# Optimization experiments

Hardware: AMD Instinct MI355X
Metric: run time of the kernel (lower is better)

The kernel has to match this reference:

```python
import jax, jax.numpy as jnp
import numpy as np

EPS = 1e-5        # torch LayerNorm default eps
INNER = 4
AFFECT_W = 0.3
BATCH = 65536
DIM = 128


def _ln(x, g, b):
    m = jnp.mean(x, axis=-1, keepdims=True)
    v = jnp.var(x, axis=-1, keepdims=True)
    return (x - m) * jax.lax.rsqrt(v + EPS) * g + b


def _gelu(x):
    return jax.nn.gelu(x, approximate=False)  # torch nn.GELU default (erf)


def setup_inputs() -> dict:
    key = jax.random.key(0)
    ks = jax.random.split(key, 18)
    B, d = BATCH, DIM

    def W(k, i, o):
        return jax.random.normal(k, (i, o), jnp.float32) / np.float32(np.sqrt(i))

    return {
        "x": jax.random.normal(ks[0], (B, d), jnp.float32),
        "y_init": jax.random.normal(ks[1], (B, d), jnp.float32),
        "affect_vec": jax.random.normal(ks[2], (B, 3), jnp.float32),
        "ln_latent_g": jnp.ones((3 * d,), jnp.float32), "ln_latent_b": jnp.zeros((3 * d,), jnp.float32),
        "ln_answer_g": jnp.ones((2 * d,), jnp.float32), "ln_answer_b": jnp.zeros((2 * d,), jnp.float32),
        "ln_z_g": jnp.ones((d,), jnp.float32), "ln_z_b": jnp.zeros((d,), jnp.float32),
        "lat_w1": W(ks[3], 3 * d, 2 * d), "lat_b1": jnp.zeros((2 * d,), jnp.float32),
        "lat_w2": W(ks[4], 2 * d, d), "lat_b2": jnp.zeros((d,), jnp.float32),
        "ans_w1": W(ks[5], 2 * d, 2 * d), "ans_b1": jnp.zeros((2 * d,), jnp.float32),
        "ans_w2": W(ks[6], 2 * d, d), "ans_b2": jnp.zeros((d,), jnp.float32),
        "aff_w": W(ks[7], 3, d), "aff_b": jnp.zeros((d,), jnp.float32),
        "gate_w": W(ks[8], 2 * d, 1), "gate_b": jnp.zeros((1,), jnp.float32),
        "q_w": W(ks[9], d, d), "q_b": jnp.zeros((d,), jnp.float32),
        "k_w": W(ks[10], d, d), "k_b": jnp.zeros((d,), jnp.float32),
        "v_w": W(ks[11], d, d), "v_b": jnp.zeros((d,), jnp.float32),
        "o_w": W(ks[12], d, d), "o_b": jnp.zeros((d,), jnp.float32),
        "pad_w1": W(ks[13], d, d // 2), "pad_b1": jnp.zeros((d // 2,), jnp.float32),
        "pad_w2": W(ks[14], d // 2, 3), "pad_b2": jnp.zeros((3,), jnp.float32),
        "K": 5,
    }


def _forward(x, y_init, affect_vec, ln_latent_g, ln_latent_b, ln_answer_g, ln_answer_b,
             ln_z_g, ln_z_b, lat_w1, lat_b1, lat_w2, lat_b2, ans_w1, ans_b1, ans_w2, ans_b2,
             aff_w, aff_b, gate_w, gate_b, q_w, q_b, k_w, k_b, v_w, v_b, o_w, o_b,
             pad_w1, pad_b1, pad_w2, pad_b2, K):
    d = x.shape[-1]
    scale = jnp.float32(d) ** -0.5
    y = y_init
    z = jnp.zeros_like(y)
    confs = []     # scalar gate means (detached, like .item() in torch)
    history = []   # list of [B, 1, d] z snapshots
    memory = []    # SoulKernel memory buffer: list of [d] rinse_state[0] snapshots
    for _ in range(K):
        for _ in range(INNER):
            li = _ln(jnp.concatenate([x, y, z], axis=-1), ln_latent_g, ln_latent_b)
            z_delta = _gelu(li @ lat_w1 + lat_b1) @ lat_w2 + lat_b2
            z = _ln(z + 0.3 * z_delta, ln_z_g, ln_z_b)
        affect_latent = jnp.tanh(affect_vec @ aff_w + aff_b)          # [B, d]
        gate = jax.nn.sigmoid(jnp.concatenate([z, affect_latent], axis=-1) @ gate_w + gate_b)  # [B, 1]
        z = z + AFFECT_W * gate * affect_latent
        confs.append(jax.lax.stop_gradient(jnp.mean(gate)))
        history.append(z[:, None, :])
        if len(history) > 1:
            seq = jnp.concatenate(history, axis=1)  # [B, t, d]
            Q = seq @ q_w + q_b
            Kt = seq @ k_w + k_b
            V = seq @ v_w + v_b
            attn = jax.nn.softmax(jnp.einsum('bsd,btd->bst', Q, Kt) * scale, axis=-1)
            attn_out = jnp.einsum('bst,btd->bsd', attn, V) @ o_w + o_b
            z = _ln(z + attn_out[:, -1, :], ln_z_g, ln_z_b)
        rinse = jnp.tanh(z + y)
        # SoulKernel (hope is computed but unused in the original)
        faith = jnp.sqrt(sum(confs) / len(confs))
        z = z + faith * 0.05 * z
        future = jnp.mean(jnp.stack(memory[-3:]), axis=0) if memory else jnp.zeros((d,), x.dtype)  # [d]
        bond = jnp.tanh(jax.lax.stop_gradient(jnp.mean(x * z)) + jax.lax.stop_gradient(jnp.mean(y * rinse)))
        z = z + 0.2 * bond * (future - z)
        rinse = jnp.tanh(rinse + future * 0.3)
        memory.append(jax.lax.stop_gradient(rinse[0]))
        ai = _ln(jnp.concatenate([y, z], axis=-1), ln_answer_g, ln_answer_b)
        y = y + 0.4 * (_gelu(ai @ ans_w1 + ans_b1) @ ans_w2 + ans_b2)
    pad = jnp.tanh(_gelu(z @ pad_w1 + pad_b1) @ pad_w2 + pad_b2)
    return y, jnp.stack(confs), pad


def reference(x, y_init, affect_vec, ln_latent_g, ln_latent_b, ln_answer_g, ln_answer_b,
              ln_z_g, ln_z_b, lat_w1, lat_b1, lat_w2, lat_b2, ans_w1, ans_b1, ans_w2, ans_b2,
              aff_w, aff_b, gate_w, gate_b, q_w, q_b, k_w, k_b, v_w, v_b, o_w, o_b,
              pad_w1, pad_b1, pad_w2, pad_b2, K):
    return _forward(x, y_init, affect_vec, ln_latent_g, ln_latent_b, ln_answer_g, ln_answer_b,
                    ln_z_g, ln_z_b, lat_w1, lat_b1, lat_w2, lat_b2, ans_w1, ans_b1, ans_w2, ans_b2,
                    aff_w, aff_b, gate_w, gate_b, q_w, q_b, k_w, k_b, v_w, v_b, o_w, o_b,
                    pad_w1, pad_b1, pad_w2, pad_b2, K)
```

## Files before the change

### kernel.cpp

```cpp
#include <hip/hip_runtime.h>
#include <math.h>


#define BATCH 65536
#define D 128
#define BD ((size_t)BATCH * D)
#define NSTEP 5
#define ROWS 32
#define NTHR 256
#define NBLK (BATCH / ROWS)
#define LN_EPS 1e-5f
#define ATT_SCALE 0.08838834764831845f
#define LDA 132
#define LDB 260

#define WS_Z    ((size_t)0)
#define WS_H1   (BD)
#define WS_PART (WS_H1 + 5*BD)
#define WS_SCAL (WS_PART + (size_t)NBLK*4)
#define WS_H2   (WS_SCAL + 2048)
#define WS_KV_END (WS_H2 + 5*BD)

#define SC_FS   0
#define SC_B02  1
#define SC_CSUM 2
#define SC_FUT  16
#define SC_MEM  256
#define SC_R10  960

struct Args {
  const float *x, *y_init, *affect;
  const float *g_lat, *b_lat, *g_ans, *b_ans, *g_z, *b_z;
  const float *lw1, *lb1, *lw2, *lb2;
  const float *aw1, *ab1, *aw2, *ab2;
  const float *affw, *affb, *gw, *gb;
  const float *qw, *qb, *kw, *kb, *vw, *vb, *ow, *ob;
  const float *pw1, *pb1, *pw2, *pb2;
  float *Y, *conf, *pad;
  float *Z, *H1, *H2, *PART, *SCAL;
  int useKV;
};

__device__ __forceinline__ float4 ld4(const float* p) { return *(const float4*)p; }
__device__ __forceinline__ void st4(float* p, float4 v) { *(float4*)p = v; }
__device__ __forceinline__ float geluf(float v) { return 0.5f*v*(1.0f + erff(v*0.70710678118654752f)); }
__device__ __forceinline__ float dot4(float4 a, float4 b){ return a.x*b.x + a.y*b.y + a.z*b.z + a.w*b.w; }
__device__ __forceinline__ void accSQ(float4 v, float& S, float& Q) {
  S += v.x+v.y+v.z+v.w;
  Q += v.x*v.x + v.y*v.y + v.z*v.z + v.w*v.w;
}

template<int KDIM, int NPT>
__device__ __forceinline__ void mm_block(const float* __restrict__ W, int N,
                                         const float* As, int lda,
                                         int rg, int cg, float (&acc)[4][NPT])
{
  const float* a0 = As + (rg*4+0)*lda;
  const float* a1 = As + (rg*4+1)*lda;
  const float* a2 = As + (rg*4+2)*lda;
  const float* a3 = As + (rg*4+3)*lda;
  const float* wp = W + cg*NPT;
  #pragma unroll 4
  for (int k = 0; k < KDIM; ++k) {
    float w[NPT];
    if constexpr (NPT == 8) {
      float4 w0 = ld4(wp + (size_t)k*N);
      float4 w1 = ld4(wp + (size_t)k*N + 4);
      w[0]=w0.x; w[1]=w0.y; w[2]=w0.z; w[3]=w0.w;
      w[4]=w1.x; w[5]=w1.y; w[6]=w1.z; w[7]=w1.w;
    } else if constexpr (NPT == 4) {
      float4 w0 = ld4(wp + (size_t)k*N);
      w[0]=w0.x; w[1]=w0.y; w[2]=w0.z; w[3]=w0.w;
    } else {
      float2 w0 = *(const float2*)(wp + (size_t)k*N);
      w[0]=w0.x; w[1]=w0.y;
    }
    float av0=a0[k], av1=a1[k], av2=a2[k], av3=a3[k];
    #pragma unroll
    for (int c = 0; c < NPT; ++c) {
      acc[0][c] += av0*w[c];
      acc[1][c] += av1*w[c];
      acc[2][c] += av2*w[c];
      acc[3][c] += av3*w[c];
    }
  }
}

__device__ __forceinline__ void z_ln_update(const Args& A, int row0, int rg, int cg,
                                            const float (&add)[4][4])
{
  float4 g4 = ld4(A.g_z + cg*4);
  float4 b4 = ld4(A.b_z + cg*4);
  #pragma unroll
  for (int rr = 0; rr < 4; ++rr) {
    size_t off = (size_t)(row0 + rg*4 + rr)*D + cg*4;
    float4 z = ld4(A.Z + off);
    float v0 = z.x + add[rr][0];
    float v1 = z.y + add[rr][1];
    float v2 = z.z + add[rr][2];
    float v3 = z.w + add[rr][3];
    float S = v0+v1+v2+v3;
    float Q = v0*v0+v1*v1+v2*v2+v3*v3;
    S += __shfl_xor(S,1);  Q += __shfl_xor(Q,1);
    S += __shfl_xor(S,2);  Q += __shfl_xor(Q,2);
    S += __shfl_xor(S,4);  Q += __shfl_xor(Q,4);
    S += __shfl_xor(S,8);  Q += __shfl_xor(Q,8);
    S += __shfl_xor(S,16); Q += __shfl_xor(Q,16);
    float m  = S*(1.f/128.f);
    float rs = rsqrtf(Q*(1.f/128.f) - m*m + LN_EPS);
    float4 o;
    o.x = (v0-m)*rs*g4.x + b4.x;
    o.y = (v1-m)*rs*g4.y + b4.y;
    o.z = (v2-m)*rs*g4.z + b4.z;
    o.w = (v3-m)*rs*g4.w + b4.w;
    st4(A.Z + off, o);
  }
}

__device__ __forceinline__ void stage_raw(float* sA, const float* src, int row0, int t)
{
  for (int e4 = t; e4 < ROWS*32; e4 += NTHR) {
    int r = e4 >> 5, c4 = e4 & 31;
    st4(sA + r*LDA + c4*4, ld4(src + (size_t)(row0+r)*D + c4*4));
  }
}

__device__ __forceinline__ void epilogue_phase(const Args& A, float* sB, float* sM, float* sR,
                                               int row0, int t, int rg, int cg, int r8, int sub)
{
  const float fs  = A.SCAL[SC_FS];
  const float b02 = A.SCAL[SC_B02];
  const float a   = fs*(1.0f - b02);
  for (int e4 = t; e4 < ROWS*32; e4 += NTHR) {
    int r = e4 >> 5, c4 = e4 & 31;
    size_t off = (size_t)(row0 + r)*D + c4*4;
    float4 z = ld4(A.Z + off);
    float4 f = ld4(A.SCAL + SC_FUT + c4*4);
    z.x = z.x*a + b02*f.x;
    z.y = z.y*a + b02*f.y;
    z.z = z.z*a + b02*f.z;
    z.w = z.w*a + b02*f.w;
    st4(A.Z + off, z);
  }
  __syncthreads();
  {
    const float* yr = A.Y + (size_t)(row0 + r8)*D;
    const float* zr = A.Z + (size_t)(row0 + r8)*D;
    float S = 0.f, Q = 0.f;
    #pragma unroll
    for (int j = 0; j < 4; ++j) {
      int c = (sub + 8*j)*4;
      accSQ(ld4(yr + c), S, Q);
      accSQ(ld4(zr + c), S, Q);
    }
    S += __shfl_xor(S,1); Q += __shfl_xor(Q,1);
    S += __shfl_xor(S,2); Q += __shfl_xor(Q,2);
    S += __shfl_xor(S,4); Q += __shfl_xor(Q,4);
    if (sub == 0) {
      float m = S*(1.f/256.f);
      sM[r8] = m;
      sR[r8] = rsqrtf(Q*(1.f/256.f) - m*m + LN_EPS);
    }
  }
  __syncthreads();
  for (int e4 = t; e4 < ROWS*64; e4 += NTHR) {
    int r = e4 >> 6, c4 = e4 & 63;
    int k = c4*4;
    float m = sM[r], rs = sR[r];
    float4 v = (k < D) ? ld4(A.Y + (size_t)(row0+r)*D + k)
                       : ld4(A.Z + (size_t)(row0+r)*D + (k - D));
    float4 g = ld4(A.g_ans + k);
    float4 b = ld4(A.b_ans + k);
    float4 o;
    o.x = (v.x-m)*rs*g.x + b.x;
    o.y = (v.y-m)*rs*g.y + b.y;
    o.z = (v.z-m)*rs*g.z + b.z;
    o.w = (v.w-m)*rs*g.w + b.w;
    st4(sB + r*LDB + k, o);
  }
  __syncthreads();
  float acc[4][8] = {};
  mm_block<256,8>(A.aw1, 256, sB, LDB, rg, cg, acc);
  float4 b1a = ld4(A.ab1 + cg*8);
  float4 b1b = ld4(A.ab1 + cg*8 + 4);
  float h[4][8];
  #pragma unroll
  for (int rr = 0; rr < 4; ++rr) {
    h[rr][0]=geluf(acc[rr][0]+b1a.x); h[rr][1]=geluf(acc[rr][1]+b1a.y);
    h[rr][2]=geluf(acc[rr][2]+b1a.z); h[rr][3]=geluf(acc[rr][3]+b1a.w);
    h[rr][4]=geluf(acc[rr][4]+b1b.x); h[rr][5]=geluf(acc[rr][5]+b1b.y);
    h[rr][6]=geluf(acc[rr][6]+b1b.z); h[rr][7]=geluf(acc[rr][7]+b1b.w);
  }
  __syncthreads();
  #pragma unroll
  for (int rr = 0; rr < 4; ++rr) {
    float4 h0; h0.x=h[rr][0]; h0.y=h[rr][1]; h0.z=h[rr][2]; h0.w=h[rr][3];
    float4 h1; h1.x=h[rr][4]; h1.y=h[rr][5]; h1.z=h[rr][6]; h1.w=h[rr][7];
    st4(sB + (rg*4+rr)*LDB + cg*8,     h0);
    st4(sB + (rg*4+rr)*LDB + cg*8 + 4, h1);
  }
  __syncthreads();
  float acc2[4][4] = {};
  mm_block<256,4>(A.aw2, 128, sB, LDB, rg, cg, acc2);
  float4 b2 = ld4(A.ab2 + cg*4);
  #pragma unroll
  for (int rr = 0; rr < 4; ++rr) {
    size_t off = (size_t)(row0 + rg*4 + rr)*D + cg*4;
    float4 y = ld4(A.Y + off);
    y.x += 0.4f*(acc2[rr][0] + b2.x);
    y.y += 0.4f*(acc2[rr][1] + b2.y);
    y.z += 0.4f*(acc2[rr][2] + b2.z);
    y.w += 0.4f*(acc2[rr][3] + b2.w);
    st4(A.Y + off, y);
  }
  __syncthreads();
}

__global__ void prepK(Args A)
{
  size_t i  = (size_t)blockIdx.x*blockDim.x + threadIdx.x;
  size_t n4 = BD/4;
  float4 zero; zero.x=0.f; zero.y=0.f; zero.z=0.f; zero.w=0.f;
  for (; i < n4; i += (size_t)gridDim.x*blockDim.x) {
    ((float4*)A.Z)[i] = zero;
    ((float4*)A.Y)[i] = ((const float4*)A.y_init)[i];
  }
}

template<int STEP>
__global__ __launch_bounds__(NTHR, 2) void stepK(Args A)
{
  __shared__ __align__(16) float sA[ROWS*LDA];
  __shared__ __align__(16) float sB[ROWS*LDB];
  __shared__ float sM[ROWS], sR[ROWS], sG[ROWS];
  __shared__ float sS[ROWS][8];
  __shared__ float sRed[4][2];

  const int t = threadIdx.x;
  const int row0 = blockIdx.x * ROWS;
  const int rg = t >> 5, cg = t & 31;
  const int r8 = t >> 3, sub = t & 7;

  if (STEP > 0)
    epilogue_phase(A, sB, sM, sR, row0, t, rg, cg, r8, sub);

  #pragma unroll 1
  for (int it = 0; it < 4; ++it) {
    {
      const float* xr = A.x + (size_t)(row0 + r8)*D;
      const float* yr = A.Y + (size_t)(row0 + r8)*D;
      const float* zr = A.Z + (size_t)(row0 + r8)*D;
      float S = 0.f, Q = 0.f;
      #pragma unroll
      for (int j = 0; j < 4; ++j) {
        int c = (sub + 8*j)*4;
        accSQ(ld4(xr + c), S, Q);
        accSQ(ld4(yr + c), S, Q);
        accSQ(ld4(zr + c), S, Q);
      }
      S += __shfl_xor(S,1); Q += __shfl_xor(Q,1);
      S += __shfl_xor(S,2); Q += __shfl_xor(Q,2);
      S += __shfl_xor(S,4); Q += __shfl_xor(Q,4);
      if (sub == 0) {
        float m = S*(1.f/384.f);
        sM[r8] = m;
        sR[r8] = rsqrtf(Q*(1.f/384.f) - m*m + LN_EPS);
      }
    }
    __syncthreads();
    float acc[4][8] = {};
    #pragma unroll 1
    for (int seg = 0; seg < 3; ++seg) {
      const float* src = (seg == 0) ? A.x : (seg == 1 ? (const float*)A.Y : (const float*)A.Z);
      for (int e4 = t; e4 < ROWS*32; e4 += NTHR) {
        int r = e4 >> 5, c4 = e4 & 31;
        float4 v = ld4(src + (size_t)(row0+r)*D + c4*4);
        float m = sM[r], rs = sR[r];
        int k = seg*D + c4*4;
        float4 g = ld4(A.g_lat + k);
        float4 b = ld4(A.b_lat + k);
        float4 o;
        o.x = (v.x-m)*rs*g.x + b.x;
        o.y = (v.y-m)*rs*g.y + b.y;
        o.z = (v.z-m)*rs*g.z + b.z;
        o.w = (v.w-m)*rs*g.w + b.w;
        st4(sA + r*LDA + c4*4, o);
      }
      __syncthreads();
      mm_block<128,8>(A.lw1 + (size_t)seg*D*256, 256, sA, LDA, rg, cg, acc);
      __syncthreads();
    }
    float4 l1a = ld4(A.lb1 + cg*8);
    float4 l1b = ld4(A.lb1 + cg*8 + 4);
    #pragma unroll
    for (int rr = 0; rr < 4; ++rr) {
      float4 h0, h1;
      h0.x = geluf(acc[rr][0]+l1a.x); h0.y = geluf(acc[rr][1]+l1a.y);
      h0.z = geluf(acc[rr][2]+l1a.z); h0.w = geluf(acc[rr][3]+l1a.w);
      h1.x = geluf(acc[rr][4]+l1b.x); h1.y = geluf(acc[rr][5]+l1b.y);
      h1.z = geluf(acc[rr][6]+l1b.z); h1.w = geluf(acc[rr][7]+l1b.w);
      st4(sB + (rg*4+rr)*LDB + cg*8,     h0);
      st4(sB + (rg*4+rr)*LDB + cg*8 + 4, h1);
    }
    __syncthreads();
    float acc2[4][4] = {};
    mm_block<256,4>(A.lw2, 128, sB, LDB, rg, cg, acc2);
    float4 l2 = ld4(A.lb2 + cg*4);
    float add[4][4];
    #pragma unroll
    for (int rr = 0; rr < 4; ++rr) {
      add[rr][0] = 0.3f*(acc2[rr][0]+l2.x);
      add[rr][1] = 0.3f*(acc2[rr][1]+l2.y);
      add[rr][2] = 0.3f*(acc2[rr][2]+l2.z);
      add[rr][3] = 0.3f*(acc2[rr][3]+l2.w);
    }
    z_ln_update(A, row0, rg, cg, add);
    __syncthreads();
  }

  {
    size_t row = (size_t)row0 + r8;
    const float* zr = A.Z + row*D;
    float af0 = A.affect[row*3+0];
    float af1 = A.affect[row*3+1];
    float af2 = A.affect[row*3+2];
    float dg = 0.f;
    #pragma unroll
    for (int j = 0; j < 4; ++j) {
      int c = (sub + 8*j)*4;
      float4 zv = ld4(zr + c);
      float4 g1 = ld4(A.gw + c);
      float4 g2 = ld4(A.gw + D + c);
      float4 w0 = ld4(A.affw + c);
      float4 w1 = ld4(A.affw + D + c);
      float4 w2 = ld4(A.affw + 2*D + c);
      float4 ab = ld4(A.affb + c);
      float4 al;
      al.x = tanhf(af0*w0.x + af1*w1.x + af2*w2.x + ab.x);
      al.y = tanhf(af0*w0.y + af1*w1.y + af2*w2.y + ab.y);
      al.z = tanhf(af0*w0.z + af1*w1.z + af2*w2.z + ab.z);
      al.w = tanhf(af0*w0.w + af1*w1.w + af2*w2.w + ab.w);
      st4(sA + r8*LDA + c, al);
      dg += dot4(zv, g1) + dot4(al, g2);
    }
    dg += __shfl_xor(dg,1);
    dg += __shfl_xor(dg,2);
    dg += __shfl_xor(dg,4);
    if (sub == 0) sG[r8] = 1.f/(1.f + expf(-(dg + A.gb[0])));
  }
  __syncthreads();
  {
    float* zhw = A.H1 + (size_t)STEP*BD;
    for (int e4 = t; e4 < ROWS*32; e4 += NTHR) {
      int r = e4 >> 5, c4 = e4 & 31;
      size_t off = (size_t)(row0+r)*D + c4*4;
      float4 z  = ld4(A.Z + off);
      float4 al = ld4(sA + r*LDA + c4*4);
      float g = 0.3f * sG[r];
      z.x += g*al.x; z.y += g*al.y; z.z += g*al.z; z.w += g*al.w;
      st4(A.Z + off, z);
      if (!A.useKV) st4(zhw + off, z);
    }
  }
  __syncthreads();

  float q[4][4];
  if (A.useKV || STEP > 0) {
    stage_raw(sA, A.Z, row0, t);
    __syncthreads();
  }
  if (A.useKV) {
    float kacc[4][4] = {}, vacc[4][4] = {};
    mm_block<128,4>(A.kw, 128, sA, LDA, rg, cg, kacc);
    mm_block<128,4>(A.vw, 128, sA, LDA, rg, cg, vacc);
    float4 kb4 = ld4(A.kb + cg*4);
    float4 vb4 = ld4(A.vb + cg*4);
    float* KH = A.H1 + (size_t)STEP*BD;
    float* VH = A.H2 + (size_t)STEP*BD;
    #pragma unroll
    for (int rr = 0; rr < 4; ++rr) {
      size_t off = (size_t)(row0 + rg*4 + rr)*D + cg*4;
      float4 kv; kv.x=kacc[rr][0]+kb4.x; kv.y=kacc[rr][1]+kb4.y;
                 kv.z=kacc[rr][2]+kb4.z; kv.w=kacc[rr][3]+kb4.w;
      float4 vv; vv.x=vacc[rr][0]+vb4.x; vv.y=vacc[rr][1]+vb4.y;
                 vv.z=vacc[rr][2]+vb4.z; vv.w=vacc[rr][3]+vb4.w;
      st4(KH + off, kv);
      st4(VH + off, vv);
    }
  }
  if (STEP > 0) {
    float qacc[4][4] = {};
    mm_block<128,4>(A.qw, 128, sA, LDA, rg, cg, qacc);
    float4 qb4 = ld4(A.qb + cg*4);
    #pragma unroll
    for (int rr = 0; rr < 4; ++rr) {
      q[rr][0]=qacc[rr][0]+qb4.x; q[rr][1]=qacc[rr][1]+qb4.y;
      q[rr][2]=qacc[rr][2]+qb4.z; q[rr][3]=qacc[rr][3]+qb4.w;
    }
  }

  if (STEP > 0) {
    if (A.useKV) {
      #pragma unroll 1
      for (int j = 0; j <= STEP; ++j) {
        const float* KH = A.H1 + (size_t)j*BD;
        #pragma unroll
        for (int rr = 0; rr < 4; ++rr) {
          float4 kv = ld4(KH + (size_t)(row0 + rg*4 + rr)*D + cg*4);
          float s = q[rr][0]*kv.x + q[rr][1]*kv.y + q[rr][2]*kv.z + q[rr][3]*kv.w;
          s += __shfl_xor(s,1); s += __shfl_xor(s,2); s += __shfl_xor(s,4);
          s += __shfl_xor(s,8); s += __shfl_xor(s,16);
          if (cg == 0) sS[rg*4+rr][j] = s;
        }
      }
    } else {
      #pragma unroll 1
      for (int j = 0; j <= STEP; ++j) {
        __syncthreads();
        stage_raw(sA, A.H1 + (size_t)j*BD, row0, t);
        __syncthreads();
        float kacc[4][4] = {};
        mm_block<128,4>(A.kw, 128, sA, LDA, rg, cg, kacc);
        float4 kb4 = ld4(A.kb + cg*4);
        #pragma unroll
        for (int rr = 0; rr < 4; ++rr) {
          float s = q[rr][0]*(kacc[rr][0]+kb4.x) + q[rr][1]*(kacc[rr][1]+kb4.y)
                  + q[rr][2]*(kacc[rr][2]+kb4.z) + q[rr][3]*(kacc[rr][3]+kb4.w);
          s += __shfl_xor(s,1); s += __shfl_xor(s,2); s += __shfl_xor(s,4);
          s += __shfl_xor(s,8); s += __shfl_xor(s,16);
          if (cg == 0) sS[rg*4+rr][j] = s;
        }
      }
    }
    __syncthreads();
    if (t < ROWS) {
      float mx = -3.0e38f;
      for (int j = 0; j <= STEP; ++j) { float v = sS[t][j]*ATT_SCALE; sS[t][j] = v; mx = fmaxf(mx, v); }
      float sum = 0.f;
      for (int j = 0; j <= STEP; ++j) { float p = expf(sS[t][j]-mx); sS[t][j] = p; sum += p; }
      float inv = 1.f/sum;
      for (int j = 0; j <= STEP; ++j) sS[t][j] *= inv;
    }
    __syncthreads();
    float ao[4][4] = {};
    if (A.useKV) {
      #pragma unroll 1
      for (int j = 0; j <= STEP; ++j) {
        const float* VH = A.H2 + (size_t)j*BD;
        #pragma unroll
        for (int rr = 0; rr < 4; ++rr) {
          float p = sS[rg*4+rr][j];
          float4 vv = ld4(VH + (size_t)(row0 + rg*4 + rr)*D + cg*4);
          ao[rr][0] += p*vv.x; ao[rr][1] += p*vv.y;
          ao[rr][2] += p*vv.z; ao[rr][3] += p*vv.w;
        }
      }
    } else {
      #pragma unroll 1
      for (int j = 0; j <= STEP; ++j) {
        __syncthreads();
        stage_raw(sA, A.H1 + (size_t)j*BD, row0, t);
        __syncthreads();
        float vacc[4][4] = {};
        mm_block<128,4>(A.vw, 128, sA, LDA, rg, cg, vacc);
        float4 vb4 = ld4(A.vb + cg*4);
        #pragma unroll
        for (int rr = 0; rr < 4; ++rr) {
          float p = sS[rg*4+rr][j];
          ao[rr][0] += p*(vacc[rr][0]+vb4.x);
          ao[rr][1] += p*(vacc[rr][1]+vb4.y);
          ao[rr][2] += p*(vacc[rr][2]+vb4.z);
          ao[rr][3] += p*(vacc[rr][3]+vb4.w);
        }
      }
      __syncthreads();
    }
    #pragma unroll
    for (int rr = 0; rr < 4; ++rr) {
      float4 v; v.x=ao[rr][0]; v.y=ao[rr][1]; v.z=ao[rr][2]; v.w=ao[rr][3];
      st4(sA + (rg*4+rr)*LDA + cg*4, v);
    }
    __syncthreads();
    float oacc[4][4] = {};
    mm_block<128,4>(A.ow, 128, sA, LDA, rg, cg, oacc);
    float4 ob4 = ld4(A.ob + cg*4);
    float add[4][4];
    #pragma unroll
    for (int rr = 0; rr < 4; ++rr) {
      add[rr][0] = oacc[rr][0]+ob4.x;
      add[rr][1] = oacc[rr][1]+ob4.y;
      add[rr][2] = oacc[rr][2]+ob4.z;
      add[rr][3] = oacc[rr][3]+ob4.w;
    }
    z_ln_update(A, row0, rg, cg, add);
    __syncthreads();
  }

  {
    float sxz = 0.f, syr = 0.f;
    for (int e4 = t; e4 < ROWS*32; e4 += NTHR) {
      int r = e4 >> 5, c4 = e4 & 31;
      size_t off = (size_t)(row0+r)*D + c4*4;
      float4 xv = ld4(A.x + off);
      float4 zv = ld4(A.Z + off);
      float4 yv = ld4(A.Y + off);
      float4 rn;
      rn.x = tanhf(zv.x + yv.x);
      rn.y = tanhf(zv.y + yv.y);
      rn.z = tanhf(zv.z + yv.z);
      rn.w = tanhf(zv.w + yv.w);
      sxz += dot4(xv, zv);
      syr += dot4(yv, rn);
      if (blockIdx.x == 0 && r == 0)
        st4(A.SCAL + SC_R10 + c4*4, rn);
    }
    #pragma unroll
    for (int m2 = 1; m2 < 64; m2 <<= 1) { sxz += __shfl_xor(sxz,m2); syr += __shfl_xor(syr,m2); }
    if ((t & 63) == 0) { sRed[t>>6][0] = sxz; sRed[t>>6][1] = syr; }
    __syncthreads();
    if (t == 0) {
      float X = 0.f, Yv = 0.f, G = 0.f;
      #pragma unroll
      for (int w2 = 0; w2 < 4; ++w2) { X += sRed[w2][0]; Yv += sRed[w2][1]; }
      #pragma unroll
      for (int r = 0; r < ROWS; ++r) G += sG[r];
      float* p = A.PART + (size_t)blockIdx.x*4;
      p[0] = G; p[1] = X; p[2] = Yv;
    }
  }
}

template<int STEP>
__global__ void redK(Args A)
{
  __shared__ float sRed[4][3];
  const int t = threadIdx.x;
  float sg = 0.f, sxz = 0.f, syr = 0.f;
  for (int b = t; b < NBLK; b += 256) {
    const float* p = A.PART + (size_t)b*4;
    sg += p[0]; sxz += p[1]; syr += p[2];
  }
  #pragma unroll
  for (int m = 1; m < 64; m <<= 1) {
    sg  += __shfl_xor(sg,m);
    sxz += __shfl_xor(sxz,m);
    syr += __shfl_xor(syr,m);
  }
  if ((t & 63) == 0) { int w = t>>6; sRed[w][0]=sg; sRed[w][1]=sxz; sRed[w][2]=syr; }
  __syncthreads();
  if (t == 0) {
    float G=0.f, X=0.f, Yv=0.f;
    #pragma unroll
    for (int w = 0; w < 4; ++w) { G += sRed[w][0]; X += sRed[w][1]; Yv += sRed[w][2]; }
    float conf = G * (1.f/(float)BATCH);
    float csum = conf + (STEP == 0 ? 0.f : A.SCAL[SC_CSUM]);
    A.SCAL[SC_CSUM] = csum;
    A.conf[STEP] = conf;
    float faith = sqrtf(csum / (float)(STEP+1));
    float fs = 1.f + 0.05f*faith;
    float bond = tanhf((fs*X + Yv) * (1.f/((float)BATCH*(float)D)));
    A.SCAL[SC_FS]  = fs;
    A.SCAL[SC_B02] = 0.2f*bond;
  }
  if (t < D) {
    float fut = 0.f;
    if (STEP > 0) {
      int lo = (STEP-3 < 0) ? 0 : STEP-3;
      float s = 0.f;
      for (int j = lo; j < STEP; ++j) s += A.SCAL[SC_MEM + j*D + t];
      fut = s / (float)(STEP - lo);
    }
    A.SCAL[SC_FUT + t] = fut;
    A.SCAL[SC_MEM + STEP*D + t] = tanhf(A.SCAL[SC_R10 + t] + 0.3f*fut);
  }
}

__global__ __launch_bounds__(NTHR, 2) void finalK(Args A)
{
  __shared__ __align__(16) float sA[ROWS*LDA];
  __shared__ __align__(16) float sB[ROWS*LDB];
  __shared__ float sM[ROWS], sR[ROWS];
  const int t = threadIdx.x;
  const int row0 = blockIdx.x * ROWS;
  const int rg = t >> 5, cg = t & 31;
  const int r8 = t >> 3, sub = t & 7;

  epilogue_phase(A, sB, sM, sR, row0, t, rg, cg, r8, sub);

  stage_raw(sA, A.Z, row0, t);
  __syncthreads();
  float acc[4][2] = {};
  mm_block<128,2>(A.pw1, 64, sA, LDA, rg, cg, acc);
  float2 pb = *(const float2*)(A.pb1 + cg*2);
  #pragma unroll
  for (int rr = 0; rr < 4; ++rr) {
    sB[(rg*4+rr)*LDB + cg*2 + 0] = geluf(acc[rr][0] + pb.x);
    sB[(rg*4+rr)*LDB + cg*2 + 1] = geluf(acc[rr][1] + pb.y);
  }
  __syncthreads();
  {
    float o0=0.f, o1=0.f, o2=0.f;
    #pragma unroll
    for (int jj = 0; jj < 8; ++jj) {
      int j = sub*8 + jj;
      float p = sB[r8*LDB + j];
      o0 += p*A.pw2[j*3+0];
      o1 += p*A.pw2[j*3+1];
      o2 += p*A.pw2[j*3+2];
    }
    o0 += __shfl_xor(o0,1); o0 += __shfl_xor(o0,2); o0 += __shfl_xor(o0,4);
    o1 += __shfl_xor(o1,1); o1 += __shfl_xor(o1,2); o1 += __shfl_xor(o1,4);
    o2 += __shfl_xor(o2,1); o2 += __shfl_xor(o2,2); o2 += __shfl_xor(o2,4);
    if (sub == 0) {
      size_t ro = (size_t)(row0 + r8)*3;
      A.pad[ro+0] = tanhf(o0 + A.pb2[0]);
      A.pad[ro+1] = tanhf(o1 + A.pb2[1]);
      A.pad[ro+2] = tanhf(o2 + A.pb2[2]);
    }
  }
}

extern "C" void kernel_launch(void* const* d_in, const int* in_sizes, int n_in,
                              void* d_out, int out_size, void* d_ws, size_t ws_size,
                              hipStream_t stream)
{
  (void)in_sizes; (void)n_in; (void)out_size;
  Args a;
  a.x      = (const float*)d_in[0];
  a.y_init = (const float*)d_in[1];
  a.affect = (const float*)d_in[2];
  a.g_lat  = (const float*)d_in[3];
  a.b_lat  = (const float*)d_in[4];
  a.g_ans  = (const float*)d_in[5];
  a.b_ans  = (const float*)d_in[6];
  a.g_z    = (const float*)d_in[7];
  a.b_z    = (const float*)d_in[8];
  a.lw1    = (const float*)d_in[9];
  a.lb1    = (const float*)d_in[10];
  a.lw2    = (const float*)d_in[11];
  a.lb2    = (const float*)d_in[12];
  a.aw1    = (const float*)d_in[13];
  a.ab1    = (const float*)d_in[14];
  a.aw2    = (const float*)d_in[15];
  a.ab2    = (const float*)d_in[16];
  a.affw   = (const float*)d_in[17];
  a.affb   = (const float*)d_in[18];
  a.gw     = (const float*)d_in[19];
  a.gb     = (const float*)d_in[20];
  a.qw     = (const float*)d_in[21];
  a.qb     = (const float*)d_in[22];
  a.kw     = (const float*)d_in[23];
  a.kb     = (const float*)d_in[24];
  a.vw     = (const float*)d_in[25];
  a.vb     = (const float*)d_in[26];
  a.ow     = (const float*)d_in[27];
  a.ob     = (const float*)d_in[28];
  a.pw1    = (const float*)d_in[29];
  a.pb1    = (const float*)d_in[30];
  a.pw2    = (const float*)d_in[31];
  a.pb2    = (const float*)d_in[32];
  float* out = (float*)d_out;
  a.Y    = out;
  a.conf = out + BD;
  a.pad  = a.conf + NSTEP;
  float* ws = (float*)d_ws;
  a.Z    = ws + WS_Z;
  a.H1   = ws + WS_H1;
  a.PART = ws + WS_PART;
  a.SCAL = ws + WS_SCAL;
  a.H2   = ws + WS_H2;
  a.useKV = (ws_size >= WS_KV_END * sizeof(float)) ? 1 : 0;

  prepK<<<dim3(2048), dim3(256), 0, stream>>>(a);
  stepK<0><<<dim3(NBLK), dim3(NTHR), 0, stream>>>(a);
  redK<0><<<dim3(1), dim3(256), 0, stream>>>(a);
  stepK<1><<<dim3(NBLK), dim3(NTHR), 0, stream>>>(a);
  redK<1><<<dim3(1), dim3(256), 0, stream>>>(a);
  stepK<2><<<dim3(NBLK), dim3(NTHR), 0, stream>>>(a);
  redK<2><<<dim3(1), dim3(256), 0, stream>>>(a);
  stepK<3><<<dim3(NBLK), dim3(NTHR), 0, stream>>>(a);
  redK<3><<<dim3(1), dim3(256), 0, stream>>>(a);
  stepK<4><<<dim3(NBLK), dim3(NTHR), 0, stream>>>(a);
  redK<4><<<dim3(1), dim3(256), 0, stream>>>(a);
  finalK<<<dim3(NBLK), dim3(NTHR), 0, stream>>>(a);
}
```

Baseline: 8.319 ms.

## Split 256-wide shared tiles into two 128-wide halves, vectorize A loads, raise occupancy

The 256-column shared buffer sB (LDB=260) is replaced by two 128-column buffers sharing one stride, so 256-K matmuls run as two 128-K passes over sA and sB. This cuts shared memory per block, and the launch bounds rise from 2 to 4 blocks per CU. The matmul inner loop now reads activations as float4 over 4 k-steps, which reduces LDS instruction count. The tighter register budget from the higher occupancy target could cause spills in the 4x8 accumulator paths.

```diff
diff --git a/kernel.cpp b/kernel.cpp
--- a/kernel.cpp
+++ b/kernel.cpp
@@ -11,8 +11,7 @@
 #define NBLK (BATCH / ROWS)
 #define LN_EPS 1e-5f
 #define ATT_SCALE 0.08838834764831845f
-#define LDA 132
-#define LDB 260
+#define LDU 132
 
 #define WS_Z    ((size_t)0)
 #define WS_H1   (BD)
@@ -49,6 +48,9 @@
   S += v.x+v.y+v.z+v.w;
   Q += v.x*v.x + v.y*v.y + v.z*v.z + v.w*v.w;
 }
+__device__ __forceinline__ float getf(const float4& v, int i) {
+  return i==0 ? v.x : (i==1 ? v.y : (i==2 ? v.z : v.w));
+}
 
 template<int KDIM, int NPT>
 __device__ __forceinline__ void mm_block(const float* __restrict__ W, int N,
@@ -60,28 +62,36 @@
   const float* a2 = As + (rg*4+2)*lda;
   const float* a3 = As + (rg*4+3)*lda;
   const float* wp = W + cg*NPT;
-  #pragma unroll 4
-  for (int k = 0; k < KDIM; ++k) {
-    float w[NPT];
-    if constexpr (NPT == 8) {
-      float4 w0 = ld4(wp + (size_t)k*N);
-      float4 w1 = ld4(wp + (size_t)k*N + 4);
-      w[0]=w0.x; w[1]=w0.y; w[2]=w0.z; w[3]=w0.w;
-      w[4]=w1.x; w[5]=w1.y; w[6]=w1.z; w[7]=w1.w;
-    } else if constexpr (NPT == 4) {
-      float4 w0 = ld4(wp + (size_t)k*N);
-      w[0]=w0.x; w[1]=w0.y; w[2]=w0.z; w[3]=w0.w;
-    } else {
-      float2 w0 = *(const float2*)(wp + (size_t)k*N);
-      w[0]=w0.x; w[1]=w0.y;
-    }
-    float av0=a0[k], av1=a1[k], av2=a2[k], av3=a3[k];
-    #pragma unroll
-    for (int c = 0; c < NPT; ++c) {
-      acc[0][c] += av0*w[c];
-      acc[1][c] += av1*w[c];
-      acc[2][c] += av2*w[c];
-      acc[3][c] += av3*w[c];
+  #pragma unroll 2
+  for (int k4 = 0; k4 < KDIM/4; ++k4) {
+    float4 av0 = ld4(a0 + k4*4);
+    float4 av1 = ld4(a1 + k4*4);
+    float4 av2 = ld4(a2 + k4*4);
+    float4 av3 = ld4(a3 + k4*4);
+    #pragma unroll
+    for (int kk = 0; kk < 4; ++kk) {
+      const int k = k4*4 + kk;
+      float w[NPT];
+      if constexpr (NPT == 8) {
+        float4 w0 = ld4(wp + (size_t)k*N);
+        float4 w1 = ld4(wp + (size_t)k*N + 4);
+        w[0]=w0.x; w[1]=w0.y; w[2]=w0.z; w[3]=w0.w;
+        w[4]=w1.x; w[5]=w1.y; w[6]=w1.z; w[7]=w1.w;
+      } else if constexpr (NPT == 4) {
+        float4 w0 = ld4(wp + (size_t)k*N);
+        w[0]=w0.x; w[1]=w0.y; w[2]=w0.z; w[3]=w0.w;
+      } else {
+        float2 w0 = *(const float2*)(wp + (size_t)k*N);
+        w[0]=w0.x; w[1]=w0.y;
+      }
+      float e0 = getf(av0,kk), e1 = getf(av1,kk), e2 = getf(av2,kk), e3 = getf(av3,kk);
+      #pragma unroll
+      for (int c = 0; c < NPT; ++c) {
+        acc[0][c] += e0*w[c];
+        acc[1][c] += e1*w[c];
+        acc[2][c] += e2*w[c];
+        acc[3][c] += e3*w[c];
+      }
     }
   }
 }
@@ -121,11 +131,12 @@
 {
   for (int e4 = t; e4 < ROWS*32; e4 += NTHR) {
     int r = e4 >> 5, c4 = e4 & 31;
-    st4(sA + r*LDA + c4*4, ld4(src + (size_t)(row0+r)*D + c4*4));
-  }
-}
-
-__device__ __forceinline__ void epilogue_phase(const Args& A, float* sB, float* sM, float* sR,
+    st4(sA + r*LDU + c4*4, ld4(src + (size_t)(row0+r)*D + c4*4));
+  }
+}
+
+__device__ __forceinline__ void epilogue_phase(const Args& A, float* sA, float* sB,
+                                               float* sM, float* sR,
                                                int row0, int t, int rg, int cg, int r8, int sub)
 {
   const float fs  = A.SCAL[SC_FS];
@@ -176,11 +187,13 @@
     o.y = (v.y-m)*rs*g.y + b.y;
     o.z = (v.z-m)*rs*g.z + b.z;
     o.w = (v.w-m)*rs*g.w + b.w;
-    st4(sB + r*LDB + k, o);
+    float* base = (k < 128) ? sA : (sB - 128);
+    st4(base + r*LDU + k, o);
   }
   __syncthreads();
   float acc[4][8] = {};
-  mm_block<256,8>(A.aw1, 256, sB, LDB, rg, cg, acc);
+  mm_block<128,8>(A.aw1,                   256, sA, LDU, rg, cg, acc);
+  mm_block<128,8>(A.aw1 + (size_t)128*256, 256, sB, LDU, rg, cg, acc);
   float4 b1a = ld4(A.ab1 + cg*8);
   float4 b1b = ld4(A.ab1 + cg*8 + 4);
   float h[4][8];
@@ -192,16 +205,20 @@
     h[rr][6]=geluf(acc[rr][6]+b1b.z); h[rr][7]=geluf(acc[rr][7]+b1b.w);
   }
   __syncthreads();
-  #pragma unroll
-  for (int rr = 0; rr < 4; ++rr) {
-    float4 h0; h0.x=h[rr][0]; h0.y=h[rr][1]; h0.z=h[rr][2]; h0.w=h[rr][3];
-    float4 h1; h1.x=h[rr][4]; h1.y=h[rr][5]; h1.z=h[rr][6]; h1.w=h[rr][7];
-    st4(sB + (rg*4+rr)*LDB + cg*8,     h0);
-    st4(sB + (rg*4+rr)*LDB + cg*8 + 4, h1);
+  {
+    float* hb = (cg < 16) ? sA : (sB - 128);
+    #pragma unroll
+    for (int rr = 0; rr < 4; ++rr) {
+      float4 h0; h0.x=h[rr][0]; h0.y=h[rr][1]; h0.z=h[rr][2]; h0.w=h[rr][3];
+      float4 h1; h1.x=h[rr][4]; h1.y=h[rr][5]; h1.z=h[rr][6]; h1.w=h[rr][7];
+      st4(hb + (rg*4+rr)*LDU + cg*8,     h0);
+      st4(hb + (rg*4+rr)*LDU + cg*8 + 4, h1);
+    }
   }
   __syncthreads();
   float acc2[4][4] = {};
-  mm_block<256,4>(A.aw2, 128, sB, LDB, rg, cg, acc2);
+  mm_block<128,4>(A.aw2,                   128, sA, LDU, rg, cg, acc2);
+  mm_block<128,4>(A.aw2 + (size_t)128*128, 128, sB, LDU, rg, cg, acc2);
   float4 b2 = ld4(A.ab2 + cg*4);
   #pragma unroll
   for (int rr = 0; rr < 4; ++rr) {
@@ -228,10 +245,10 @@
 }
 
 template<int STEP>
-__global__ __launch_bounds__(NTHR, 2) void stepK(Args A)
-{
-  __shared__ __align__(16) float sA[ROWS*LDA];
-  __shared__ __align__(16) float sB[ROWS*LDB];
+__global__ __launch_bounds__(NTHR, 4) void stepK(Args A)
+{
+  __shared__ __align__(16) float sA[ROWS*LDU];
+  __shared__ __align__(16) float sB[ROWS*LDU];
   __shared__ float sM[ROWS], sR[ROWS], sG[ROWS];
   __shared__ float sS[ROWS][8];
   __shared__ float sRed[4][2];
@@ -242,7 +259,7 @@
   const int r8 = t >> 3, sub = t & 7;
 
   if (STEP > 0)
-    epilogue_phase(A, sB, sM, sR, row0, t, rg, cg, r8, sub);
+    epilogue_phase(A, sA, sB, sM, sR, row0, t, rg, cg, r8, sub);
 
   #pragma unroll 1
   for (int it = 0; it < 4; ++it) {
@@ -284,27 +301,31 @@
         o.y = (v.y-m)*rs*g.y + b.y;
         o.z = (v.z-m)*rs*g.z + b.z;
         o.w = (v.w-m)*rs*g.w + b.w;
-        st4(sA + r*LDA + c4*4, o);
+        st4(sA + r*LDU + c4*4, o);
       }
       __syncthreads();
-      mm_block<128,8>(A.lw1 + (size_t)seg*D*256, 256, sA, LDA, rg, cg, acc);
+      mm_block<128,8>(A.lw1 + (size_t)seg*D*256, 256, sA, LDU, rg, cg, acc);
       __syncthreads();
     }
     float4 l1a = ld4(A.lb1 + cg*8);
     float4 l1b = ld4(A.lb1 + cg*8 + 4);
-    #pragma unroll
-    for (int rr = 0; rr < 4; ++rr) {
-      float4 h0, h1;
-      h0.x = geluf(acc[rr][0]+l1a.x); h0.y = geluf(acc[rr][1]+l1a.y);
-      h0.z = geluf(acc[rr][2]+l1a.z); h0.w = geluf(acc[rr][3]+l1a.w);
-      h1.x = geluf(acc[rr][4]+l1b.x); h1.y = geluf(acc[rr][5]+l1b.y);
-      h1.z = geluf(acc[rr][6]+l1b.z); h1.w = geluf(acc[rr][7]+l1b.w);
-      st4(sB + (rg*4+rr)*LDB + cg*8,     h0);
-      st4(sB + (rg*4+rr)*LDB + cg*8 + 4, h1);
+    {
+      float* hb = (cg < 16) ? sA : (sB - 128);
+      #pragma unroll
+      for (int rr = 0; rr < 4; ++rr) {
+        float4 h0, h1;
+        h0.x = geluf(acc[rr][0]+l1a.x); h0.y = geluf(acc[rr][1]+l1a.y);
+        h0.z = geluf(acc[rr][2]+l1a.z); h0.w = geluf(acc[rr][3]+l1a.w);
+        h1.x = geluf(acc[rr][4]+l1b.x); h1.y = geluf(acc[rr][5]+l1b.y);
+        h1.z = geluf(acc[rr][6]+l1b.z); h1.w = geluf(acc[rr][7]+l1b.w);
+        st4(hb + (rg*4+rr)*LDU + cg*8,     h0);
+        st4(hb + (rg*4+rr)*LDU + cg*8 + 4, h1);
+      }
     }
     __syncthreads();
     float acc2[4][4] = {};
-    mm_block<256,4>(A.lw2, 128, sB, LDB, rg, cg, acc2);
+    mm_block<128,4>(A.lw2,                   128, sA, LDU, rg, cg, acc2);
+    mm_block<128,4>(A.lw2 + (size_t)128*128, 128, sB, LDU, rg, cg, acc2);
     float4 l2 = ld4(A.lb2 + cg*4);
     float add[4][4];
     #pragma unroll
@@ -340,7 +361,7 @@
       al.y = tanhf(af0*w0.y + af1*w1.y + af2*w2.y + ab.y);
       al.z = tanhf(af0*w0.z + af1*w1.z + af2*w2.z + ab.z);
       al.w = tanhf(af0*w0.w + af1*w1.w + af2*w2.w + ab.w);
-      st4(sA + r8*LDA + c, al);
+      st4(sA + r8*LDU + c, al);
       dg += dot4(zv, g1) + dot4(al, g2);
     }
     dg += __shfl_xor(dg,1);
@@ -355,7 +376,7 @@
       int r = e4 >> 5, c4 = e4 & 31;
       size_t off = (size_t)(row0+r)*D + c4*4;
       float4 z  = ld4(A.Z + off);
-      float4 al = ld4(sA + r*LDA + c4*4);
+      float4 al = ld4(sA + r*LDU + c4*4);
       float g = 0.3f * sG[r];
       z.x += g*al.x; z.y += g*al.y; z.z += g*al.z; z.w += g*al.w;
       st4(A.Z + off, z);
@@ -371,8 +392,8 @@
   }
   if (A.useKV) {
     float kacc[4][4] = {}, vacc[4][4] = {};
-    mm_block<128,4>(A.kw, 128, sA, LDA, rg, cg, kacc);
-    mm_block<128,4>(A.vw, 128, sA, LDA, rg, cg, vacc);
+    mm_block<128,4>(A.kw, 128, sA, LDU, rg, cg, kacc);
+    mm_block<128,4>(A.vw, 128, sA, LDU, rg, cg, vacc);
     float4 kb4 = ld4(A.kb + cg*4);
     float4 vb4 = ld4(A.vb + cg*4);
     float* KH = A.H1 + (size_t)STEP*BD;
@@ -390,7 +411,7 @@
   }
   if (STEP > 0) {
     float qacc[4][4] = {};
-    mm_block<128,4>(A.qw, 128, sA, LDA, rg, cg, qacc);
+    mm_block<128,4>(A.qw, 128, sA, LDU, rg, cg, qacc);
     float4 qb4 = ld4(A.qb + cg*4);
     #pragma unroll
     for (int rr = 0; rr < 4; ++rr) {
@@ -420,7 +441,7 @@
         stage_raw(sA, A.H1 + (size_t)j*BD, row0, t);
         __syncthreads();
         float kacc[4][4] = {};
-        mm_block<128,4>(A.kw, 128, sA, LDA, rg, cg, kacc);
+        mm_block<128,4>(A.kw, 128, sA, LDU, rg, cg, kacc);
         float4 kb4 = ld4(A.kb + cg*4);
         #pragma unroll
         for (int rr = 0; rr < 4; ++rr) {
@@ -462,7 +483,7 @@
         stage_raw(sA, A.H1 + (size_t)j*BD, row0, t);
         __syncthreads();
         float vacc[4][4] = {};
-        mm_block<128,4>(A.vw, 128, sA, LDA, rg, cg, vacc);
+        mm_block<128,4>(A.vw, 128, sA, LDU, rg, cg, vacc);
         float4 vb4 = ld4(A.vb + cg*4);
         #pragma unroll
         for (int rr = 0; rr < 4; ++rr) {
@@ -478,11 +499,11 @@
     #pragma unroll
     for (int rr = 0; rr < 4; ++rr) {
       float4 v; v.x=ao[rr][0]; v.y=ao[rr][1]; v.z=ao[rr][2]; v.w=ao[rr][3];
-      st4(sA + (rg*4+rr)*LDA + cg*4, v);
+      st4(sA + (rg*4+rr)*LDU + cg*4, v);
     }
     __syncthreads();
     float oacc[4][4] = {};
-    mm_block<128,4>(A.ow, 128, sA, LDA, rg, cg, oacc);
+    mm_block<128,4>(A.ow, 128, sA, LDU, rg, cg, oacc);
     float4 ob4 = ld4(A.ob + cg*4);
     float add[4][4];
     #pragma unroll
@@ -575,27 +596,27 @@
   }
 }
 
-__global__ __launch_bounds__(NTHR, 2) void finalK(Args A)
-{
-  __shared__ __align__(16) float sA[ROWS*LDA];
-  __shared__ __align__(16) float sB[ROWS*LDB];
+__global__ __launch_bounds__(NTHR, 4) void finalK(Args A)
+{
+  __shared__ __align__(16) float sA[ROWS*LDU];
+  __shared__ __align__(16) float sB[ROWS*LDU];
   __shared__ float sM[ROWS], sR[ROWS];
   const int t = threadIdx.x;
   const int row0 = blockIdx.x * ROWS;
   const int rg = t >> 5, cg = t & 31;
   const int r8 = t >> 3, sub = t & 7;
 
-  epilogue_phase(A, sB, sM, sR, row0, t, rg, cg, r8, sub);
+  epilogue_phase(A, sA, sB, sM, sR, row0, t, rg, cg, r8, sub);
 
   stage_raw(sA, A.Z, row0, t);
   __syncthreads();
   float acc[4][2] = {};
-  mm_block<128,2>(A.pw1, 64, sA, LDA, rg, cg, acc);
+  mm_block<128,2>(A.pw1, 64, sA, LDU, rg, cg, acc);
   float2 pb = *(const float2*)(A.pb1 + cg*2);
   #pragma unroll
   for (int rr = 0; rr < 4; ++rr) {
-    sB[(rg*4+rr)*LDB + cg*2 + 0] = geluf(acc[rr][0] + pb.x);
-    sB[(rg*4+rr)*LDB + cg*2 + 1] = geluf(acc[rr][1] + pb.y);
+    sB[(rg*4+rr)*LDU + cg*2 + 0] = geluf(acc[rr][0] + pb.x);
+    sB[(rg*4+rr)*LDU + cg*2 + 1] = geluf(acc[rr][1] + pb.y);
   }
   __syncthreads();
   {
@@ -603,7 +624,7 @@
     #pragma unroll
     for (int jj = 0; jj < 8; ++jj) {
       int j = sub*8 + jj;
-      float p = sB[r8*LDB + j];
+      float p = sB[r8*LDU + j];
       o0 += p*A.pw2[j*3+0];
       o1 += p*A.pw2[j*3+1];
       o2 += p*A.pw2[j*3+2];
```

After: 8.452 ms. About the same (+1.6%).
